# Optimization experiments

Hardware: AMD Instinct MI355X
Metric: run time of the kernel (lower is better)

## Reference

```python
import jax, jax.numpy as jnp
import numpy as np

N, C, H = 256, 128, 4
D = C // H


def setup_inputs() -> dict:
    key = jax.random.key(0)
    ks = jax.random.split(key, 7)
    pair_rep = jax.random.normal(ks[0], (N, N, C), dtype=jnp.float32)
    distance_matrix = jax.random.normal(ks[1], (N, N), dtype=jnp.float32)
    Wqkv = jax.random.normal(ks[2], (C, 3 * C), dtype=jnp.float32) * (1.0 / np.sqrt(C))
    bqkv = jax.random.normal(ks[3], (3 * C,), dtype=jnp.float32) * 0.02
    Wout = jax.random.normal(ks[4], (C, C), dtype=jnp.float32) * (1.0 / np.sqrt(C))
    bout = jax.random.normal(ks[5], (C,), dtype=jnp.float32) * 0.02
    dscale = jnp.ones((1,), dtype=jnp.float32)
    mask = jax.random.randint(ks[6], (N, N), 0, 2).astype(jnp.bool_)
    return {"pair_rep": pair_rep, "distance_matrix": distance_matrix, "Wqkv": Wqkv,
            "bqkv": bqkv, "Wout": Wout, "bout": bout, "dscale": dscale, "mask": mask}


def reference(pair_rep, distance_matrix, Wqkv, bqkv, Wout, bout, dscale, mask):
    n = pair_rep.shape[0]
    qkv = pair_rep @ Wqkv + bqkv                      # [n,n,3c]
    q, k, v = jnp.split(qkv, 3, axis=-1)
    q = q.reshape(n, n, H, D)
    k = k.reshape(n, n, H, D)
    v = v.reshape(n, n, H, D)
    # scores[h,i,j,k] = q[i,j,h,:] . k[i,k,h,:] / sqrt(D)
    scores = jnp.einsum('ijhd,ikhd->hijk', q, k) / np.sqrt(D)
    bias = (dscale[0] * distance_matrix)[None, None, :, :]   # [1,1,n,n]
    scores = scores + bias
    scores = jnp.where(mask[None, None, :, :], -jnp.inf, scores)
    attn = jax.nn.softmax(scores, axis=-1)            # [H,n,n,n]
    out = jnp.einsum('hijk,ikhd->ijhd', attn, v).reshape(n, n, C)
    return out @ Wout + bout
```

## Files before the change

kernel.cpp:

```cpp
#include <hip/hip_runtime.h>
#include <hip/hip_bf16.h>
#include <math.h>

#define NN 256
#define CC 128
#define HH 4
#define DD 32

typedef uint4 u128;
typedef __bf16 bf16x8 __attribute__((ext_vector_type(8)));
typedef float f32x4 __attribute__((ext_vector_type(4)));

#define LOG2E 1.4426950408889634f
#define QSC (0.17677669529663687f * LOG2E)

__global__ __launch_bounds__(256) void prep_kernel(
    const float* __restrict__ dm, const int* __restrict__ mask,
    const float* __restrict__ dscale,
    const float* __restrict__ Wqkv, const float* __restrict__ Wout,
    const float* __restrict__ pair,
    float* __restrict__ biasM,
    __hip_bfloat16* __restrict__ Wt_qkv, __hip_bfloat16* __restrict__ Wt_out,
    __hip_bfloat16* __restrict__ Abf)
{
    const int b = blockIdx.x, t = threadIdx.x;
    if (b < 256) {
        int idx = b * 256 + t;
        biasM[idx] = mask[idx] ? -INFINITY : dscale[0] * dm[idx] * LOG2E;
    } else if (b < 448) {
        int idx = (b - 256) * 256 + t;
        int n = idx >> 7, k = idx & 127;
        Wt_qkv[idx] = __float2bfloat16(Wqkv[(size_t)k * 384 + n]);
    } else if (b < 512) {
        int idx = (b - 448) * 256 + t;
        int n = idx >> 7, k = idx & 127;
        Wt_out[idx] = __float2bfloat16(Wout[(size_t)k * CC + n]);
    } else {
        size_t e = (size_t)(b - 512) * 2048 + (size_t)t * 8;
        float4 v0 = *(const float4*)(pair + e);
        float4 v1 = *(const float4*)(pair + e + 4);
        __hip_bfloat162 a01 = __float22bfloat162_rn(float2{v0.x, v0.y});
        __hip_bfloat162 a23 = __float22bfloat162_rn(float2{v0.z, v0.w});
        __hip_bfloat162 a45 = __float22bfloat162_rn(float2{v1.x, v1.y});
        __hip_bfloat162 a67 = __float22bfloat162_rn(float2{v1.z, v1.w});
        u128 pk;
        pk.x = *(unsigned int*)&a01;
        pk.y = *(unsigned int*)&a23;
        pk.z = *(unsigned int*)&a45;
        pk.w = *(unsigned int*)&a67;
        *(u128*)&Abf[e] = pk;
    }
}

__global__ __launch_bounds__(512, 4) void qkv_mfma_kernel(
    const __hip_bfloat16* __restrict__ A,
    const __hip_bfloat16* __restrict__ Bt,
    const float* __restrict__ bias,
    __hip_bfloat16* __restrict__ out)
{
    __shared__ __align__(16) __hip_bfloat16 As[128][136];
    __shared__ __align__(16) __hip_bfloat16 Bs[96][136];
    const int t = threadIdx.x;
    const int m0 = blockIdx.x * 128;
    const int n0 = blockIdx.y * 96;

    #pragma unroll
    for (int it = 0; it < 4; ++it) {
        int idx = it * 512 + t;
        int r = idx >> 4, c8 = (idx & 15) * 8;
        *(u128*)&As[r][c8] = *(const u128*)(A + (size_t)(m0 + r) * CC + c8);
    }
    #pragma unroll
    for (int it = 0; it < 3; ++it) {
        int idx = it * 512 + t;
        int n = idx >> 4, c8 = (idx & 15) * 8;
        *(u128*)&Bs[n][c8] = *(const u128*)(Bt + (size_t)(n0 + n) * CC + c8);
    }
    __syncthreads();

    const int w = t >> 6, lane = t & 63;
    const int n16 = lane & 15, quad = lane >> 4;
    const int mw = (w & 3) * 32, nw = (w >> 2) * 48;

    bf16x8 pf[2][4];
    #pragma unroll
    for (int mt = 0; mt < 2; ++mt)
        #pragma unroll
        for (int ks = 0; ks < 4; ++ks)
            pf[mt][ks] = *(const bf16x8*)&As[mw + mt * 16 + n16][ks * 32 + quad * 8];

    f32x4 acc[2][3];
    #pragma unroll
    for (int mt = 0; mt < 2; ++mt)
        #pragma unroll
        for (int nt = 0; nt < 3; ++nt) acc[mt][nt] = (f32x4){0.f, 0.f, 0.f, 0.f};

    #pragma unroll
    for (int nt = 0; nt < 3; ++nt) {
        bf16x8 wf[4];
        #pragma unroll
        for (int ks = 0; ks < 4; ++ks)
            wf[ks] = *(const bf16x8*)&Bs[nw + nt * 16 + n16][ks * 32 + quad * 8];
        #pragma unroll
        for (int ks = 0; ks < 4; ++ks)
            #pragma unroll
            for (int mt = 0; mt < 2; ++mt)
                acc[mt][nt] = __builtin_amdgcn_mfma_f32_16x16x32_bf16(wf[ks], pf[mt][ks], acc[mt][nt], 0, 0, 0);
    }

    #pragma unroll
    for (int nt = 0; nt < 3; ++nt) {
        int nbase = n0 + nw + nt * 16 + quad * 4;
        float4 b4 = *(const float4*)(bias + nbase);
        float sc = (nbase < CC) ? QSC : 1.0f;
        #pragma unroll
        for (int mt = 0; mt < 2; ++mt) {
            int m = m0 + mw + mt * 16 + n16;
            __hip_bfloat162 h01 = __float22bfloat162_rn(float2{(acc[mt][nt][0] + b4.x) * sc, (acc[mt][nt][1] + b4.y) * sc});
            __hip_bfloat162 h23 = __float22bfloat162_rn(float2{(acc[mt][nt][2] + b4.z) * sc, (acc[mt][nt][3] + b4.w) * sc});
            uint2 pk;
            pk.x = *(unsigned int*)&h01;
            pk.y = *(unsigned int*)&h23;
            *(uint2*)&out[(size_t)m * 384 + nbase] = pk;
        }
    }
}

__global__ __launch_bounds__(512, 4) void attn_mfma_kernel(
    const __hip_bfloat16* __restrict__ qkv,
    const float* __restrict__ biasM,
    __hip_bfloat16* __restrict__ attn_out)
{
    __shared__ __align__(16) __hip_bfloat16 Ks[NN][40];
    __shared__ __align__(16) __hip_bfloat16 VTs[DD][264];
    __shared__ __align__(16) __hip_bfloat16 Ps[8][16][136];

    const int bi = blockIdx.x;
    const int i = bi >> 2, h = bi & 3;
    const int t = threadIdx.x;

    {
        const int r = t >> 1, half = t & 1;
        const __hip_bfloat16* base = qkv + (size_t)(i * NN + r) * 384 + h * DD;
        const u128* ksrc = (const u128*)(base + CC) + half * 2;
        u128* kdst = (u128*)&Ks[r][0] + half * 2;
        kdst[0] = ksrc[0];
        kdst[1] = ksrc[1];
        const u128* vsrc = (const u128*)(base + 2 * CC) + half * 2;
        u128 vr[2];
        vr[0] = vsrc[0];
        vr[1] = vsrc[1];
        const __hip_bfloat16* vh = (const __hip_bfloat16*)vr;
        #pragma unroll
        for (int dd = 0; dd < 16; ++dd) VTs[half * 16 + dd][r] = vh[dd];
    }
    __syncthreads();

    const int w = t >> 6, lane = t & 63;
    const int n16 = lane & 15, quad = lane >> 4;

    for (int jt = 0; jt < 2; ++jt) {
        const int j0 = w * 32 + jt * 16;
        const int j = j0 + n16;

        bf16x8 qa = *(const bf16x8*)(qkv + (size_t)(i * NN + j) * 384 + h * DD + quad * 8);
        const float4* brow = (const float4*)(biasM + (size_t)j * NN);

        f32x4 s[16];
        #pragma unroll
        for (int kt = 0; kt < 16; ++kt) {
            float4 b4 = brow[kt * 4 + quad];
            s[kt] = (f32x4){b4.x, b4.y, b4.z, b4.w};
        }
        __builtin_amdgcn_s_setprio(1);
        #pragma unroll
        for (int kt = 0; kt < 16; ++kt) {
            bf16x8 kb = *(const bf16x8*)&Ks[kt * 16 + n16][quad * 8];
            s[kt] = __builtin_amdgcn_mfma_f32_16x16x32_bf16(kb, qa, s[kt], 0, 0, 0);
        }
        __builtin_amdgcn_s_setprio(0);

        f32x4 sm = {0.f, 0.f, 0.f, 0.f};
        f32x4 o[2] = {(f32x4){0.f, 0.f, 0.f, 0.f}, (f32x4){0.f, 0.f, 0.f, 0.f}};
        #pragma unroll
        for (int pass = 0; pass < 2; ++pass) {
            #pragma unroll
            for (int kt8 = 0; kt8 < 8; ++kt8) {
                int kt = pass * 8 + kt8;
                float p0 = __builtin_amdgcn_exp2f(s[kt][0]);
                float p1 = __builtin_amdgcn_exp2f(s[kt][1]);
                float p2 = __builtin_amdgcn_exp2f(s[kt][2]);
                float p3 = __builtin_amdgcn_exp2f(s[kt][3]);
                sm[0] += p0; sm[1] += p1; sm[2] += p2; sm[3] += p3;
                __hip_bfloat162 h01 = __float22bfloat162_rn(float2{p0, p1});
                __hip_bfloat162 h23 = __float22bfloat162_rn(float2{p2, p3});
                uint2 pk;
                pk.x = *(unsigned int*)&h01;
                pk.y = *(unsigned int*)&h23;
                *(uint2*)&Ps[w][n16][kt8 * 16 + quad * 4] = pk;
            }
            __builtin_amdgcn_s_setprio(1);
            #pragma unroll
            for (int c = 0; c < 4; ++c) {
                bf16x8 pa = *(const bf16x8*)&Ps[w][n16][c * 32 + quad * 8];
                #pragma unroll
                for (int dt = 0; dt < 2; ++dt) {
                    bf16x8 vb = *(const bf16x8*)&VTs[dt * 16 + n16][pass * 128 + c * 32 + quad * 8];
                    o[dt] = __builtin_amdgcn_mfma_f32_16x16x32_bf16(vb, pa, o[dt], 0, 0, 0);
                }
            }
            __builtin_amdgcn_s_setprio(0);
        }
        float sum = (sm[0] + sm[1]) + (sm[2] + sm[3]);
        sum += __shfl_xor(sum, 16);
        sum += __shfl_xor(sum, 32);
        float inv = 1.0f / sum;

        __hip_bfloat16* obase = attn_out + (size_t)(i * NN + j) * CC + h * DD + quad * 4;
        #pragma unroll
        for (int dt = 0; dt < 2; ++dt) {
            __hip_bfloat162 h01 = __float22bfloat162_rn(float2{o[dt][0] * inv, o[dt][1] * inv});
            __hip_bfloat162 h23 = __float22bfloat162_rn(float2{o[dt][2] * inv, o[dt][3] * inv});
            uint2 pk;
            pk.x = *(unsigned int*)&h01;
            pk.y = *(unsigned int*)&h23;
            *(uint2*)(obase + dt * 16) = pk;
        }
    }
}

__global__ __launch_bounds__(512, 4) void out_mfma_kernel(
    const __hip_bfloat16* __restrict__ A,
    const __hip_bfloat16* __restrict__ Bt,
    const float* __restrict__ bias,
    float* __restrict__ out)
{
    __shared__ __align__(16) __hip_bfloat16 As[128][136];
    __shared__ __align__(16) __hip_bfloat16 Bs[128][136];
    const int t = threadIdx.x;
    const int m0 = blockIdx.x * 128;

    #pragma unroll
    for (int it = 0; it < 4; ++it) {
        int idx = it * 512 + t;
        int r = idx >> 4, c8 = (idx & 15) * 8;
        *(u128*)&As[r][c8] = *(const u128*)(A + (size_t)(m0 + r) * CC + c8);
    }
    #pragma unroll
    for (int it = 0; it < 4; ++it) {
        int idx = it * 512 + t;
        int n = idx >> 4, c8 = (idx & 15) * 8;
        *(u128*)&Bs[n][c8] = *(const u128*)(Bt + (size_t)n * CC + c8);
    }
    __syncthreads();

    const int w = t >> 6, lane = t & 63;
    const int n16 = lane & 15, quad = lane >> 4;
    const int mw = (w & 3) * 32, nw = (w >> 2) * 64;

    bf16x8 pf[2][4];
    #pragma unroll
    for (int mt = 0; mt < 2; ++mt)
        #pragma unroll
        for (int ks = 0; ks < 4; ++ks)
            pf[mt][ks] = *(const bf16x8*)&As[mw + mt * 16 + n16][ks * 32 + quad * 8];

    f32x4 acc[2][4];
    #pragma unroll
    for (int mt = 0; mt < 2; ++mt)
        #pragma unroll
        for (int nt = 0; nt < 4; ++nt) acc[mt][nt] = (f32x4){0.f, 0.f, 0.f, 0.f};

    #pragma unroll
    for (int nt = 0; nt < 4; ++nt) {
        bf16x8 wf[4];
        #pragma unroll
        for (int ks = 0; ks < 4; ++ks)
            wf[ks] = *(const bf16x8*)&Bs[nw + nt * 16 + n16][ks * 32 + quad * 8];
        #pragma unroll
        for (int ks = 0; ks < 4; ++ks)
            #pragma unroll
            for (int mt = 0; mt < 2; ++mt)
                acc[mt][nt] = __builtin_amdgcn_mfma_f32_16x16x32_bf16(wf[ks], pf[mt][ks], acc[mt][nt], 0, 0, 0);
    }

    #pragma unroll
    for (int nt = 0; nt < 4; ++nt) {
        int nbase = nw + nt * 16 + quad * 4;
        float4 b4 = *(const float4*)(bias + nbase);
        #pragma unroll
        for (int mt = 0; mt < 2; ++mt) {
            int m = m0 + mw + mt * 16 + n16;
            float4 ov;
            ov.x = acc[mt][nt][0] + b4.x;
            ov.y = acc[mt][nt][1] + b4.y;
            ov.z = acc[mt][nt][2] + b4.z;
            ov.w = acc[mt][nt][3] + b4.w;
            *(float4*)&out[(size_t)m * CC + nbase] = ov;
        }
    }
}

extern "C" void kernel_launch(void* const* d_in, const int* in_sizes, int n_in,
                              void* d_out, int out_size, void* d_ws, size_t ws_size,
                              hipStream_t stream) {
    const float* pair_rep = (const float*)d_in[0];
    const float* dm       = (const float*)d_in[1];
    const float* Wqkv     = (const float*)d_in[2];
    const float* bqkv     = (const float*)d_in[3];
    const float* Wout     = (const float*)d_in[4];
    const float* bout     = (const float*)d_in[5];
    const float* dscale   = (const float*)d_in[6];
    const int*   mask     = (const int*)d_in[7];
    float* out = (float*)d_out;

    char* p = (char*)d_ws;
    float* biasM = (float*)p;                 p += (size_t)NN * NN * 4;
    __hip_bfloat16* Wt_qkv = (__hip_bfloat16*)p;  p += (size_t)384 * CC * 2;
    __hip_bfloat16* Wt_out = (__hip_bfloat16*)p;  p += (size_t)CC * CC * 2;
    __hip_bfloat16* qkv  = (__hip_bfloat16*)p;    p += (size_t)65536 * 384 * 2;
    __hip_bfloat16* attn = (__hip_bfloat16*)p;
    __hip_bfloat16* Abf  = attn;

    prep_kernel<<<dim3(4608), dim3(256), 0, stream>>>(dm, mask, dscale, Wqkv, Wout, pair_rep, biasM, Wt_qkv, Wt_out, Abf);
    qkv_mfma_kernel<<<dim3(512, 4), dim3(512), 0, stream>>>(Abf, Wt_qkv, bqkv, qkv);
    attn_mfma_kernel<<<dim3(1024), dim3(512), 0, stream>>>(qkv, biasM, attn);
    out_mfma_kernel<<<dim3(512), dim3(512), 0, stream>>>(attn, Wt_out, bout, out);
}
```

Baseline: 169.7 us.

## Keep softmax probabilities in registers by permuting V layout, removing P shared staging

The attention kernel now feeds the QK^T MFMA output straight into the PV MFMA as its A operand. To make this legal it stores V transposed with a permuted key index, so the register layout of exp(scores) matches the MFMA operand layout. This drops the per-wave Ps shared-memory buffer and its write/read round trip. It also interleaves score, exp and PV work per 32-key chunk instead of holding all 16 score tiles, and raises the occupancy hint to 8 blocks per SM. The risk is register pressure under the tighter launch bound and correctness of the index permutation.

```diff
diff --git a/kernel.cpp b/kernel.cpp
--- a/kernel.cpp
+++ b/kernel.cpp
@@ -126,14 +126,13 @@
     }
 }
 
-__global__ __launch_bounds__(512, 4) void attn_mfma_kernel(
+__global__ __launch_bounds__(512, 8) void attn_mfma_kernel(
     const __hip_bfloat16* __restrict__ qkv,
     const float* __restrict__ biasM,
     __hip_bfloat16* __restrict__ attn_out)
 {
     __shared__ __align__(16) __hip_bfloat16 Ks[NN][40];
     __shared__ __align__(16) __hip_bfloat16 VTs[DD][264];
-    __shared__ __align__(16) __hip_bfloat16 Ps[8][16][136];
 
     const int bi = blockIdx.x;
     const int i = bi >> 2, h = bi & 3;
@@ -151,14 +150,16 @@
         vr[0] = vsrc[0];
         vr[1] = vsrc[1];
         const __hip_bfloat16* vh = (const __hip_bfloat16*)vr;
-        #pragma unroll
-        for (int dd = 0; dd < 16; ++dd) VTs[half * 16 + dd][r] = vh[dd];
+        const int pr = (r & ~0x1F) | ((r & 0xC) << 1) | ((r & 0x10) >> 2) | (r & 0x3);
+        #pragma unroll
+        for (int dd = 0; dd < 16; ++dd) VTs[half * 16 + dd][pr] = vh[dd];
     }
     __syncthreads();
 
     const int w = t >> 6, lane = t & 63;
     const int n16 = lane & 15, quad = lane >> 4;
 
+    #pragma unroll
     for (int jt = 0; jt < 2; ++jt) {
         const int j0 = w * 32 + jt * 16;
         const int j = j0 + n16;
@@ -166,65 +167,71 @@
         bf16x8 qa = *(const bf16x8*)(qkv + (size_t)(i * NN + j) * 384 + h * DD + quad * 8);
         const float4* brow = (const float4*)(biasM + (size_t)j * NN);
 
-        f32x4 s[16];
-        #pragma unroll
-        for (int kt = 0; kt < 16; ++kt) {
-            float4 b4 = brow[kt * 4 + quad];
-            s[kt] = (f32x4){b4.x, b4.y, b4.z, b4.w};
-        }
-        __builtin_amdgcn_s_setprio(1);
-        #pragma unroll
-        for (int kt = 0; kt < 16; ++kt) {
-            bf16x8 kb = *(const bf16x8*)&Ks[kt * 16 + n16][quad * 8];
-            s[kt] = __builtin_amdgcn_mfma_f32_16x16x32_bf16(kb, qa, s[kt], 0, 0, 0);
-        }
-        __builtin_amdgcn_s_setprio(0);
-
         f32x4 sm = {0.f, 0.f, 0.f, 0.f};
-        f32x4 o[2] = {(f32x4){0.f, 0.f, 0.f, 0.f}, (f32x4){0.f, 0.f, 0.f, 0.f}};
-        #pragma unroll
-        for (int pass = 0; pass < 2; ++pass) {
-            #pragma unroll
-            for (int kt8 = 0; kt8 < 8; ++kt8) {
-                int kt = pass * 8 + kt8;
-                float p0 = __builtin_amdgcn_exp2f(s[kt][0]);
-                float p1 = __builtin_amdgcn_exp2f(s[kt][1]);
-                float p2 = __builtin_amdgcn_exp2f(s[kt][2]);
-                float p3 = __builtin_amdgcn_exp2f(s[kt][3]);
-                sm[0] += p0; sm[1] += p1; sm[2] += p2; sm[3] += p3;
-                __hip_bfloat162 h01 = __float22bfloat162_rn(float2{p0, p1});
-                __hip_bfloat162 h23 = __float22bfloat162_rn(float2{p2, p3});
-                uint2 pk;
-                pk.x = *(unsigned int*)&h01;
-                pk.y = *(unsigned int*)&h23;
-                *(uint2*)&Ps[w][n16][kt8 * 16 + quad * 4] = pk;
-            }
-            __builtin_amdgcn_s_setprio(1);
-            #pragma unroll
-            for (int c = 0; c < 4; ++c) {
-                bf16x8 pa = *(const bf16x8*)&Ps[w][n16][c * 32 + quad * 8];
-                #pragma unroll
-                for (int dt = 0; dt < 2; ++dt) {
-                    bf16x8 vb = *(const bf16x8*)&VTs[dt * 16 + n16][pass * 128 + c * 32 + quad * 8];
-                    o[dt] = __builtin_amdgcn_mfma_f32_16x16x32_bf16(vb, pa, o[dt], 0, 0, 0);
-                }
-            }
-            __builtin_amdgcn_s_setprio(0);
-        }
+        f32x4 o0 = {0.f, 0.f, 0.f, 0.f}, o1 = {0.f, 0.f, 0.f, 0.f};
+
+        #pragma unroll 2
+        for (int c = 0; c < 8; ++c) {
+            float4 b0 = brow[c * 8 + quad];
+            float4 b1 = brow[c * 8 + 4 + quad];
+            bf16x8 kb0 = *(const bf16x8*)&Ks[c * 32 + n16][quad * 8];
+            bf16x8 kb1 = *(const bf16x8*)&Ks[c * 32 + 16 + n16][quad * 8];
+            f32x4 s0 = __builtin_amdgcn_mfma_f32_16x16x32_bf16(
+                kb0, qa, (f32x4){b0.x, b0.y, b0.z, b0.w}, 0, 0, 0);
+            f32x4 s1 = __builtin_amdgcn_mfma_f32_16x16x32_bf16(
+                kb1, qa, (f32x4){b1.x, b1.y, b1.z, b1.w}, 0, 0, 0);
+
+            float p0 = __builtin_amdgcn_exp2f(s0[0]);
+            float p1 = __builtin_amdgcn_exp2f(s0[1]);
+            float p2 = __builtin_amdgcn_exp2f(s0[2]);
+            float p3 = __builtin_amdgcn_exp2f(s0[3]);
+            float p4 = __builtin_amdgcn_exp2f(s1[0]);
+            float p5 = __builtin_amdgcn_exp2f(s1[1]);
+            float p6 = __builtin_amdgcn_exp2f(s1[2]);
+            float p7 = __builtin_amdgcn_exp2f(s1[3]);
+            sm[0] += p0 + p4;
+            sm[1] += p1 + p5;
+            sm[2] += p2 + p6;
+            sm[3] += p3 + p7;
+
+            __hip_bfloat162 q01 = __float22bfloat162_rn(float2{p0, p1});
+            __hip_bfloat162 q23 = __float22bfloat162_rn(float2{p2, p3});
+            __hip_bfloat162 q45 = __float22bfloat162_rn(float2{p4, p5});
+            __hip_bfloat162 q67 = __float22bfloat162_rn(float2{p6, p7});
+            u128 pk;
+            pk.x = *(unsigned int*)&q01;
+            pk.y = *(unsigned int*)&q23;
+            pk.z = *(unsigned int*)&q45;
+            pk.w = *(unsigned int*)&q67;
+            bf16x8 pa = *(bf16x8*)&pk;
+
+            bf16x8 vb0 = *(const bf16x8*)&VTs[n16][c * 32 + quad * 8];
+            bf16x8 vb1 = *(const bf16x8*)&VTs[16 + n16][c * 32 + quad * 8];
+            o0 = __builtin_amdgcn_mfma_f32_16x16x32_bf16(vb0, pa, o0, 0, 0, 0);
+            o1 = __builtin_amdgcn_mfma_f32_16x16x32_bf16(vb1, pa, o1, 0, 0, 0);
+        }
+
         float sum = (sm[0] + sm[1]) + (sm[2] + sm[3]);
         sum += __shfl_xor(sum, 16);
         sum += __shfl_xor(sum, 32);
         float inv = 1.0f / sum;
 
         __hip_bfloat16* obase = attn_out + (size_t)(i * NN + j) * CC + h * DD + quad * 4;
-        #pragma unroll
-        for (int dt = 0; dt < 2; ++dt) {
-            __hip_bfloat162 h01 = __float22bfloat162_rn(float2{o[dt][0] * inv, o[dt][1] * inv});
-            __hip_bfloat162 h23 = __float22bfloat162_rn(float2{o[dt][2] * inv, o[dt][3] * inv});
+        {
+            __hip_bfloat162 h01 = __float22bfloat162_rn(float2{o0[0] * inv, o0[1] * inv});
+            __hip_bfloat162 h23 = __float22bfloat162_rn(float2{o0[2] * inv, o0[3] * inv});
             uint2 pk;
             pk.x = *(unsigned int*)&h01;
             pk.y = *(unsigned int*)&h23;
-            *(uint2*)(obase + dt * 16) = pk;
+            *(uint2*)(obase) = pk;
+        }
+        {
+            __hip_bfloat162 h01 = __float22bfloat162_rn(float2{o1[0] * inv, o1[1] * inv});
+            __hip_bfloat162 h23 = __float22bfloat162_rn(float2{o1[2] * inv, o1[3] * inv});
+            uint2 pk;
+            pk.x = *(unsigned int*)&h01;
+            pk.y = *(unsigned int*)&h23;
+            *(uint2*)(obase + 16) = pk;
         }
     }
 }
```

New measurement: 167.2 us. No clear change (-1.5%).
